# Kernel tuning notes

Hardware: AMD Instinct MI355X
Metric: run time of the kernel (lower is better)

## Reference

```python
import jax, jax.numpy as jnp
import numpy as np

DIM = 512
H = 8
HD = DIM // H
MAX_DIST = 128
TABLE = (2 * MAX_DIST + 1) ** 2
LAMBDA_INIT = 0.8


def setup_inputs() -> dict:
    key = jax.random.key(0)
    ks = jax.random.split(key, 20)
    B, Nq, Nkv = 4, 1024, 1024
    inp = {
        "x_q": jax.random.normal(ks[0], (B, Nq, DIM), jnp.float32),
        "x_kv": jax.random.normal(ks[1], (B, Nkv, DIM), jnp.float32),
        "coords_q": jax.random.randint(ks[2], (B, Nq, 2), 0, 256, jnp.int32),
        "coords_k": jax.random.randint(ks[3], (B, Nkv, 2), 0, 256, jnp.int32),
        "alpha_map": jax.random.uniform(ks[4], (B, Nq, 1), jnp.float32),
        "Wq": jax.random.normal(ks[5], (DIM, DIM), jnp.float32) * 0.02,
        "bq": jnp.zeros((DIM,), jnp.float32),
        "Wk": jax.random.normal(ks[6], (DIM, DIM), jnp.float32) * 0.02,
        "bk": jnp.zeros((DIM,), jnp.float32),
        "Wv": jax.random.normal(ks[7], (DIM, DIM), jnp.float32) * 0.02,
        "bv": jnp.zeros((DIM,), jnp.float32),
        "lambda_q1": jax.random.normal(ks[8], (H // 2, HD), jnp.float32) * 0.1,
        "lambda_k1": jax.random.normal(ks[9], (H // 2, HD), jnp.float32) * 0.1,
        "lambda_q2": jax.random.normal(ks[10], (H // 2, HD), jnp.float32) * 0.1,
        "lambda_k2": jax.random.normal(ks[11], (H // 2, HD), jnp.float32) * 0.1,
        "rpe_table": jax.random.normal(ks[12], (TABLE, H), jnp.float32) * 0.02,
        "Wp": jax.random.normal(ks[13], (DIM, DIM), jnp.float32) * 0.02,
        "bp": jnp.zeros((DIM,), jnp.float32),
    }
    return inp


def reference(x_q, x_kv, coords_q, coords_k, alpha_map,
              Wq, bq, Wk, bk, Wv, bv,
              lambda_q1, lambda_k1, lambda_q2, lambda_k2,
              rpe_table, Wp, bp):
    B, Nq, C = x_q.shape
    Nkv = x_kv.shape[1]
    n_half = H // 2
    scale = HD ** -0.5

    # projections -> [B, H, N, HD]
    q = (x_q @ Wq.T + bq).reshape(B, Nq, H, HD).transpose(0, 2, 1, 3)
    k = (x_kv @ Wk.T + bk).reshape(B, Nkv, H, HD).transpose(0, 2, 1, 3)
    v = (x_kv @ Wv.T + bv).reshape(B, Nkv, H, HD).transpose(0, 2, 1, 3)

    # sparse relative position bias: gather per-pair from table
    rel = coords_q[:, :, None, :] - coords_k[:, None, :, :] + MAX_DIST  # [B,Nq,Nkv,2]
    rel = jnp.clip(rel, 0, 2 * MAX_DIST)
    idx = rel[..., 0] * (2 * MAX_DIST + 1) + rel[..., 1]  # [B,Nq,Nkv]
    bias = rpe_table[idx].transpose(0, 3, 1, 2)  # [B,H,Nq,Nkv]

    scores = jnp.einsum('bhqd,bhkd->bhqk', q, k) * scale + bias
    probs = jax.nn.softmax(scores, axis=-1)
    x_std = jnp.einsum('bhqk,bhkd->bhqd', probs, v)

    lam1 = jnp.exp(jnp.sum(lambda_q1 * lambda_k1, axis=-1))  # [n_half]
    lam2 = jnp.exp(jnp.sum(lambda_q2 * lambda_k2, axis=-1))
    lam = (lam1 - lam2 + LAMBDA_INIT)[None, :, None, None]

    attn_diff = probs[:, :n_half] - lam * probs[:, n_half:]
    x_diff = jnp.einsum('bhqk,bhkd->bhqd', attn_diff, v[:, :n_half])

    alpha = alpha_map[:, None]  # [B,1,Nq,1]
    x1 = x_std[:, :n_half] + alpha * x_diff
    x = jnp.concatenate([x1, x_std[:, n_half:]], axis=1)  # [B,H,Nq,HD]
    x = x.transpose(0, 2, 1, 3).reshape(B, Nq, C)
    return x @ Wp.T + bp
```

## Files before the change

kernel.cpp:

```cpp
#include <hip/hip_runtime.h>
#include <cstddef>
#include <cstdint>

#define DIM   512
#define NSEQ  1024
#define NB    4
#define LOG2E 1.44269504f

typedef unsigned short u16;
typedef short bf16x8 __attribute__((ext_vector_type(8)));
typedef _Float16 half8v __attribute__((ext_vector_type(8)));
typedef float f32x4  __attribute__((ext_vector_type(4)));

#define MFMA(a, b, c)  __builtin_amdgcn_mfma_f32_16x16x32_bf16(a, b, c, 0, 0, 0)
#define MFMAH(a, b, c) __builtin_amdgcn_mfma_f32_16x16x32_f16(a, b, c, 0, 0, 0)

__device__ inline void split2(float x, u16& h, u16& l) {
  unsigned u = __float_as_uint(x);
  unsigned hb = (u + 0x7fffu + ((u >> 16) & 1u)) >> 16;
  float fh = __uint_as_float(hb << 16);
  float r = x - fh;
  unsigned v = __float_as_uint(r);
  unsigned lb = (v + 0x7fffu + ((v >> 16) & 1u)) >> 16;
  h = (u16)hb; l = (u16)lb;
}

__device__ inline uint2 pack4(const u16 a[4]) {
  return make_uint2((unsigned)a[0] | ((unsigned)a[1] << 16),
                    (unsigned)a[2] | ((unsigned)a[3] << 16));
}

__device__ inline u16 f2h(float x) {
  _Float16 h = (_Float16)x;
  u16 r; __builtin_memcpy(&r, &h, 2);
  return r;
}
__device__ inline float h2f(u16 b) {
  _Float16 h; __builtin_memcpy(&h, &b, 2);
  return (float)h;
}
__device__ inline unsigned pkh2(float a, float b) {
  return (unsigned)f2h(a) | ((unsigned)f2h(b) << 16);
}

__device__ inline void split_body(const float* __restrict__ in,
                                  u16* __restrict__ out, int e4) {
  const int e = e4 * 4;
  const int m = e >> 9, c = e & 511;
  const float4 v = *(const float4*)(in + e);
  u16 h[4], l[4];
  split2(v.x, h[0], l[0]); split2(v.y, h[1], l[1]);
  split2(v.z, h[2], l[2]); split2(v.w, h[3], l[3]);
  u16* o = out + (size_t)m * 1024 + c;
  *(uint2*)o = pack4(h);
  *(uint2*)(o + 512) = pack4(l);
}

#define GLDS(g, l)                                                        \
  __builtin_amdgcn_global_load_lds(                                       \
      (const __attribute__((address_space(1))) void*)(g),                 \
      (__attribute__((address_space(3))) void*)(l), 16, 0, 0)

__global__ __launch_bounds__(256) void prep(
    const float* __restrict__ wq, const float* __restrict__ wk,
    const float* __restrict__ wv, const float* __restrict__ wp,
    const float* __restrict__ xq, const float* __restrict__ xkv,
    const int* __restrict__ cq, const int* __restrict__ ck,
    const float* __restrict__ rpe,
    u16* __restrict__ w2, u16* __restrict__ xq2, u16* __restrict__ xkv2,
    u16* __restrict__ biasT) {
  __shared__ u16 Ts[8 * 16 * 64];
  const int id = blockIdx.x;
  const int t = threadIdx.x;
  if (id < 1024) {
    const int y = id >> 8;
    const float* src = (y == 0) ? wq : (y == 1) ? wk : (y == 2) ? wv : wp;
    split_body(src, w2 + (size_t)y * 524288, (id & 255) * 256 + t);
  } else if (id < 5120) {
    const int e = id - 1024;
    const int y = e >> 11;
    split_body(y ? xkv : xq, y ? xkv2 : xq2, (e & 2047) * 256 + t);
  } else {
    const int e = id - 5120;
    const int q0 = (e & 15) * 64, k0 = ((e >> 4) & 63) * 16, b = e >> 10;
    const int qn = t & 63, kb = t >> 6;
    const int2 cqv = ((const int2*)cq)[b * NSEQ + q0 + qn];
#pragma unroll
    for (int j = 0; j < 4; ++j) {
      const int k = kb * 4 + j;
      const int2 ckv = ((const int2*)ck)[b * NSEQ + k0 + k];
      const int r0 = min(max(cqv.x - ckv.x + 128, 0), 256);
      const int r1 = min(max(cqv.y - ckv.y + 128, 0), 256);
      const float* rp = rpe + (size_t)(r0 * 257 + r1) * 8;
      const float4 f0 = *(const float4*)rp;
      const float4 f1 = *(const float4*)(rp + 4);
      u16* dst = Ts + k * 64 + qn;
      dst[0 * 1024] = f2h(f0.x * LOG2E); dst[1 * 1024] = f2h(f0.y * LOG2E);
      dst[2 * 1024] = f2h(f0.z * LOG2E); dst[3 * 1024] = f2h(f0.w * LOG2E);
      dst[4 * 1024] = f2h(f1.x * LOG2E); dst[5 * 1024] = f2h(f1.y * LOG2E);
      dst[6 * 1024] = f2h(f1.z * LOG2E); dst[7 * 1024] = f2h(f1.w * LOG2E);
    }
    __syncthreads();
#pragma unroll
    for (int i = 0; i < 4; ++i) {
      const int e2 = i * 256 + t;
      const int row = e2 >> 3, c8 = e2 & 7;
      const int hh = row >> 4, k = row & 15;
      const uint4 v = *(const uint4*)(Ts + row * 64 + c8 * 8);
      *(uint4*)(biasT + ((size_t)(b * 8 + hh) * 1024 + k0 + k) * 1024 +
                q0 + c8 * 8) = v;
    }
  }
}

template <int OUT_MODE>
__device__ __forceinline__ void gemm128(
    u16* __restrict__ Ah, u16* __restrict__ Al,
    u16* __restrict__ Bh, u16* __restrict__ Bl,
    const u16* __restrict__ A2, const u16* __restrict__ B2,
    const float* __restrict__ bias, void* __restrict__ outp,
    float scale, int m0, int n0) {
  const int tid = threadIdx.x;
  const int lane = tid & 63, w = tid >> 6;
  const int wm = (w & 1) * 64, wn = (w >> 1) * 32;
  const int lr = lane >> 3;
  const int scc = (lane & 7) ^ lr;

  const u16* gA = A2 + (size_t)(m0 + w * 32 + lr) * 1024 + scc * 8;
  const u16* gB = B2 + (size_t)(n0 + w * 16 + lr) * 1024 + scc * 8;
  char* lAh = (char*)Ah + w * 4096;  char* lAl = (char*)Al + w * 4096;
  char* lBh = (char*)Bh + w * 2048;  char* lBl = (char*)Bl + w * 2048;

  const int fr = lane & 15, kq = lane >> 4, fx = fr & 7;
  int aoff[2][4], boff[2][2];
#pragma unroll
  for (int s = 0; s < 2; ++s) {
#pragma unroll
    for (int i = 0; i < 4; ++i)
      aoff[s][i] = (wm + i * 16 + fr) * 64 + (((s * 4 + kq) ^ fx)) * 8;
#pragma unroll
    for (int j = 0; j < 2; ++j)
      boff[s][j] = (wn + j * 16 + fr) * 64 + (((s * 4 + kq) ^ fx)) * 8;
  }

  f32x4 acc[4][2] = {};
  for (int k0 = 0; k0 < 512; k0 += 64) {
    __syncthreads();
#pragma unroll
    for (int i = 0; i < 4; ++i) {
      GLDS(gA + (size_t)i * 8192 + k0, lAh + i * 1024);
      GLDS(gA + (size_t)i * 8192 + 512 + k0, lAl + i * 1024);
    }
#pragma unroll
    for (int i = 0; i < 2; ++i) {
      GLDS(gB + (size_t)i * 8192 + k0, lBh + i * 1024);
      GLDS(gB + (size_t)i * 8192 + 512 + k0, lBl + i * 1024);
    }
    __syncthreads();
#pragma unroll
    for (int s = 0; s < 2; ++s) {
      bf16x8 ah[4], al[4], bh[2], bl[2];
#pragma unroll
      for (int i = 0; i < 4; ++i) {
        ah[i] = *(const bf16x8*)(Ah + aoff[s][i]);
        al[i] = *(const bf16x8*)(Al + aoff[s][i]);
      }
#pragma unroll
      for (int j = 0; j < 2; ++j) {
        bh[j] = *(const bf16x8*)(Bh + boff[s][j]);
        bl[j] = *(const bf16x8*)(Bl + boff[s][j]);
      }
#pragma unroll
      for (int i = 0; i < 4; ++i)
#pragma unroll
        for (int j = 0; j < 2; ++j) {
          acc[i][j] = MFMA(al[i], bh[j], acc[i][j]);
          acc[i][j] = MFMA(ah[i], bl[j], acc[i][j]);
          acc[i][j] = MFMA(ah[i], bh[j], acc[i][j]);
        }
    }
  }

  const int er = (lane >> 4) * 4, ec = lane & 15;
#pragma unroll
  for (int i = 0; i < 4; ++i)
#pragma unroll
    for (int j = 0; j < 2; ++j) {
      const int row = m0 + wm + i * 16 + er;
      const int col = n0 + wn + j * 16 + ec;
      const float bv = bias[col];
      if (OUT_MODE == 4) {
        u16 hf[4];
#pragma unroll
        for (int r = 0; r < 4; ++r) hf[r] = f2h((acc[i][j][r] + bv) * scale);
        const int bb = row >> 10, kk = row & 1023;
        *(uint2*)((u16*)outp + ((size_t)(bb * 512 + col)) * 1024 + kk) =
            pack4(hf);
      } else {
#pragma unroll
        for (int r = 0; r < 4; ++r) {
          const float v = (acc[i][j][r] + bv) * scale;
          if (OUT_MODE == 3)
            ((u16*)outp)[(size_t)(row + r) * 512 + col] = f2h(v);
          else
            ((float*)outp)[(size_t)(row + r) * 512 + col] = v;
        }
      }
    }
}

__global__ __launch_bounds__(256, 3) void gemm_qkv(
    const u16* __restrict__ xq2, const u16* __restrict__ xkv2,
    const u16* __restrict__ w2, const float* __restrict__ bq,
    const float* __restrict__ bk, const float* __restrict__ bv,
    u16* __restrict__ q2f, u16* __restrict__ k2f, u16* __restrict__ vtf) {
  __shared__ __align__(16) u16 Ah[8192], Al[8192], Bh[4096], Bl[4096];
  const int z = blockIdx.z;
  const int m0 = blockIdx.x * 128, n0 = blockIdx.y * 64;
  if (z == 0)
    gemm128<3>(Ah, Al, Bh, Bl, xq2, w2, bq, q2f, 0.125f * LOG2E, m0, n0);
  else if (z == 1)
    gemm128<3>(Ah, Al, Bh, Bl, xkv2, w2 + 524288, bk, k2f, 1.0f, m0, n0);
  else
    gemm128<4>(Ah, Al, Bh, Bl, xkv2, w2 + 2 * 524288, bv, vtf, 1.0f, m0, n0);
}

__global__ __launch_bounds__(256, 3) void gemm_out(
    const u16* __restrict__ xa2, const u16* __restrict__ w2p,
    const float* __restrict__ bp, float* __restrict__ out) {
  __shared__ __align__(16) u16 Ah[8192], Al[8192], Bh[4096], Bl[4096];
  gemm128<0>(Ah, Al, Bh, Bl, xa2, w2p, bp, out, 1.0f,
             blockIdx.x * 128, blockIdx.y * 64);
}

__global__ __launch_bounds__(256) void attn_f16(
    const u16* __restrict__ q2f, const u16* __restrict__ k2f,
    const u16* __restrict__ vtf, const float* __restrict__ amap,
    const float* __restrict__ lq1, const float* __restrict__ lk1,
    const float* __restrict__ lq2, const float* __restrict__ lk2,
    const u16* __restrict__ biasT, u16* __restrict__ xo) {
  __shared__ __align__(16) u16 KsL[2][8192];
  __shared__ __align__(16) u16 VtL[2][8192];
  __shared__ float lam_s;

  const int tid = threadIdx.x;
  const int lane = tid & 63, w = tid >> 6;
  const int h = w >> 1, qs = w & 1;
  const int hp = blockIdx.y, b = blockIdx.z;
  const int q0 = blockIdx.x * 32;
  const int head = hp + 4 * h;
  const int lq = lane & 15, lg = lane >> 4;
  const int q = qs * 16 + lq;
  const size_t qrow = (size_t)(b * NSEQ + q0 + q);

  if (tid < 64) {
    float p1 = lq1[hp * 64 + tid] * lk1[hp * 64 + tid];
    float p2 = lq2[hp * 64 + tid] * lk2[hp * 64 + tid];
#pragma unroll
    for (int m = 32; m >= 1; m >>= 1) {
      p1 += __shfl_xor(p1, m, 64);
      p2 += __shfl_xor(p2, m, 64);
    }
    if (tid == 0) lam_s = __expf(p1) - __expf(p2) + 0.8f;
  }

  const float alpha = amap[qrow];

  half8v Qf[2];
#pragma unroll
  for (int ks = 0; ks < 2; ++ks)
    Qf[ks] = *(const half8v*)(q2f + qrow * 512 + head * 64 + ks * 32 + lg * 8);

  f32x4 Ya[4] = {};
  f32x4 Yb[4] = {};
  float m_run = -1e30f, l_run = 0.0f;

  const int lr = lane >> 3;
  const int scc = (lane & 7) ^ lr;
  const int cw = w * 4;

  auto stage = [&](int it, int p) {
#pragma unroll
    for (int i = 0; i < 4; ++i) {
      const int c = cw + i;
      const int row = c * 8 + lr;
      const int sh = row >> 6, k = row & 63;
      const u16* src = k2f + (size_t)(b * NSEQ + it * 64 + k) * 512 +
                       (hp + 4 * sh) * 64 + scc * 8;
      GLDS(src, (char*)KsL[p] + c * 1024);
    }
#pragma unroll
    for (int i = 0; i < 4; ++i) {
      const int c = cw + i;
      const int row = c * 8 + lr;
      const int hv = row >> 6, d = row & 63;
      const u16* src = vtf + (size_t)(b * 512 + (hp + 4 * hv) * 64 + d) * 1024 +
                       it * 64 + scc * 8;
      GLDS(src, (char*)VtL[p] + c * 1024);
    }
  };

  const u16* bT = biasT + ((size_t)(b * 8 + head) << 20) + q0 + q;
  auto loadBias = [&](int it, u16* rb) {
    const u16* bt = bT + (size_t)(it * 64) * 1024;
#pragma unroll
    for (int kt = 0; kt < 4; ++kt)
#pragma unroll
      for (int r = 0; r < 4; ++r)
        rb[kt * 4 + r] = bt[(size_t)(kt * 16 + lg * 4 + r) * 1024];
  };

  u16 rbA[16], rbB[16];
  stage(0, 0);
  loadBias(0, rbA);

  auto body = [&](int it, u16* rbCur, u16* rbNext) {
    const int p = it & 1;
    __syncthreads();
    if (it + 1 < 16) { stage(it + 1, p ^ 1); loadBias(it + 1, rbNext); }

    const u16* Kb = KsL[p];
    f32x4 st[4] = {};
#pragma unroll
    for (int kt = 0; kt < 4; ++kt) {
      const int krow = kt * 16 + lq;
      const int rx = krow & 7;
#pragma unroll
      for (int ks = 0; ks < 2; ++ks) {
        const int phys = (ks * 4 + lg) ^ rx;
        const half8v kf =
            *(const half8v*)(Kb + (h * 64 + krow) * 64 + phys * 8);
        st[kt] = MFMAH(kf, Qf[ks], st[kt]);
      }
    }

    float sv[4][4];
    float mx = -1e30f;
#pragma unroll
    for (int kt = 0; kt < 4; ++kt)
#pragma unroll
      for (int r = 0; r < 4; ++r) {
        const float s = st[kt][r] + h2f(rbCur[kt * 4 + r]);
        sv[kt][r] = s;
        mx = fmaxf(mx, s);
      }
    mx = fmaxf(mx, __shfl_xor(mx, 16, 64));
    mx = fmaxf(mx, __shfl_xor(mx, 32, 64));
    const float mnew = fmaxf(m_run, mx);
    const float a = exp2f(m_run - mnew);
    m_run = mnew;
    float pr[4][4], ps = 0.0f;
#pragma unroll
    for (int kt = 0; kt < 4; ++kt)
#pragma unroll
      for (int r = 0; r < 4; ++r) {
        pr[kt][r] = exp2f(sv[kt][r] - mnew);
        ps += pr[kt][r];
      }
    ps += __shfl_xor(ps, 16, 64);
    ps += __shfl_xor(ps, 32, 64);
    l_run = l_run * a + ps;
#pragma unroll
    for (int dt = 0; dt < 4; ++dt) Ya[dt] *= a;
    if (h == 1) {
#pragma unroll
      for (int dt = 0; dt < 4; ++dt) Yb[dt] *= a;
    }

    unsigned pk[4][2];
#pragma unroll
    for (int kt = 0; kt < 4; ++kt) {
      pk[kt][0] = pkh2(pr[kt][0], pr[kt][1]);
      pk[kt][1] = pkh2(pr[kt][2], pr[kt][3]);
    }
    const int srcA = lq + ((lg & 1) << 5);
    const bool t2 = lg >= 2;
    half8v pb[2];
#pragma unroll
    for (int kg = 0; kg < 2; ++kg) {
      const int k0i = kg * 2, k1i = kg * 2 + 1;
      const unsigned A0 = __shfl((int)pk[k0i][0], srcA);
      const unsigned A1 = __shfl((int)pk[k0i][1], srcA);
      const unsigned B0 = __shfl((int)pk[k1i][0], srcA);
      const unsigned B1 = __shfl((int)pk[k1i][1], srcA);
      const unsigned C0 = __shfl((int)pk[k0i][0], srcA + 16);
      const unsigned C1 = __shfl((int)pk[k0i][1], srcA + 16);
      const unsigned D0 = __shfl((int)pk[k1i][0], srcA + 16);
      const unsigned D1 = __shfl((int)pk[k1i][1], srcA + 16);
      const uint4 Pu = make_uint4(t2 ? B0 : A0, t2 ? B1 : A1,
                                  t2 ? D0 : C0, t2 ? D1 : C1);
      __builtin_memcpy(&pb[kg], &Pu, 16);
    }

    const u16* Vb = VtL[p];
#pragma unroll
    for (int kg = 0; kg < 2; ++kg) {
      if (h == 0) {
#pragma unroll
        for (int dt = 0; dt < 4; ++dt) {
          const int d = dt * 16 + lq;
          const int phys = (kg * 4 + lg) ^ (d & 7);
          const half8v v1 = *(const half8v*)(Vb + d * 64 + phys * 8);
          Ya[dt] = MFMAH(v1, pb[kg], Ya[dt]);
        }
      } else {
#pragma unroll
        for (int dt = 0; dt < 4; ++dt) {
          const int d = dt * 16 + lq;
          const int phys = (kg * 4 + lg) ^ (d & 7);
          const half8v v1 = *(const half8v*)(Vb + d * 64 + phys * 8);
          Yb[dt] = MFMAH(v1, pb[kg], Yb[dt]);
          const half8v v2 = *(const half8v*)(Vb + (64 + d) * 64 + phys * 8);
          Ya[dt] = MFMAH(v2, pb[kg], Ya[dt]);
        }
      }
    }
  };

  for (int it2 = 0; it2 < 16; it2 += 2) {
    body(it2, rbA, rbB);
    body(it2 + 1, rbB, rbA);
  }

  __syncthreads();
  float* y2x = (float*)VtL;
  float* l2s = (float*)KsL;
  if (h == 1) {
    if (lane < 16) l2s[qs * 16 + lane] = l_run;
#pragma unroll
    for (int dt = 0; dt < 4; ++dt)
#pragma unroll
      for (int r = 0; r < 4; ++r)
        y2x[(qs * 64 + lane) * 16 + dt * 4 + r] = Yb[dt][r];
  }
  __syncthreads();
  if (h == 1) {
    const float inv2 = 1.0f / l_run;
#pragma unroll
    for (int dt = 0; dt < 4; ++dt) {
      u16 hh[4], ll[4];
#pragma unroll
      for (int r = 0; r < 4; ++r) split2(Ya[dt][r] * inv2, hh[r], ll[r]);
      u16* o = xo + qrow * 1024 + (hp + 4) * 64 + dt * 16 + lg * 4;
      *(uint2*)o = pack4(hh);
      *(uint2*)(o + 512) = pack4(ll);
    }
  } else {
    const float inv1 = 1.0f / l_run;
    const float inv2 = 1.0f / l2s[qs * 16 + lq];
    const float c1 = (1.0f + alpha) * inv1;
    const float c2 = alpha * lam_s * inv2;
#pragma unroll
    for (int dt = 0; dt < 4; ++dt) {
      u16 hh[4], ll[4];
#pragma unroll
      for (int r = 0; r < 4; ++r) {
        const float y2 = y2x[(qs * 64 + lane) * 16 + dt * 4 + r];
        split2(c1 * Ya[dt][r] - c2 * y2, hh[r], ll[r]);
      }
      u16* o = xo + qrow * 1024 + hp * 64 + dt * 16 + lg * 4;
      *(uint2*)o = pack4(hh);
      *(uint2*)(o + 512) = pack4(ll);
    }
  }
}

extern "C" void kernel_launch(void* const* d_in, const int* in_sizes, int n_in,
                              void* d_out, int out_size, void* d_ws, size_t ws_size,
                              hipStream_t stream) {
  const float* x_q   = (const float*)d_in[0];
  const float* x_kv  = (const float*)d_in[1];
  const int*   c_q   = (const int*)d_in[2];
  const int*   c_k   = (const int*)d_in[3];
  const float* alpha = (const float*)d_in[4];
  const float* Wq    = (const float*)d_in[5];
  const float* bq    = (const float*)d_in[6];
  const float* Wk    = (const float*)d_in[7];
  const float* bk    = (const float*)d_in[8];
  const float* Wv    = (const float*)d_in[9];
  const float* bv    = (const float*)d_in[10];
  const float* lq1   = (const float*)d_in[11];
  const float* lk1   = (const float*)d_in[12];
  const float* lq2   = (const float*)d_in[13];
  const float* lk2   = (const float*)d_in[14];
  const float* rpe   = (const float*)d_in[15];
  const float* Wp    = (const float*)d_in[16];
  const float* bp    = (const float*)d_in[17];

  u16* w2    = (u16*)d_ws;
  u16* xq2   = (u16*)((char*)d_ws + (4u << 20));
  u16* q2f   = (u16*)((char*)d_ws + (12u << 20));
  u16* k2f   = (u16*)((char*)d_ws + (16u << 20));
  u16* vtf   = (u16*)((char*)d_ws + (20u << 20));
  u16* xa    = xq2;
  u16* biasT = (u16*)((char*)d_ws + (28u << 20));
  u16* xkv2  = (u16*)d_out;

  prep<<<9216, 256, 0, stream>>>(Wq, Wk, Wv, Wp, x_q, x_kv, c_q, c_k, rpe,
                                 w2, xq2, xkv2, biasT);
  gemm_qkv<<<dim3(32, 8, 3), 256, 0, stream>>>(xq2, xkv2, w2, bq, bk, bv,
                                               q2f, k2f, vtf);
  attn_f16<<<dim3(32, 4, NB), 256, 0, stream>>>(
      q2f, k2f, vtf, alpha, lq1, lk1, lq2, lk2, biasT, xa);
  gemm_out<<<dim3(32, 8), 256, 0, stream>>>(xa, w2 + 3 * 524288, bp,
                                            (float*)d_out);
}
```

Baseline: 210.3 us.

## Split attention KV range across two warp groups with flash-decode style merge

The attention kernel doubles its block to 512 threads and gives each half of the key sequence to a separate group of four waves. Each group runs online softmax over 32-key tiles, and the partial max, sum and output accumulators are then merged through shared memory before the final differential combine. The aim is more waves per block to hide latency and a shorter serial loop per wave. In exchange it adds a merge step with extra syncs, and it drops the bias register prefetch, so bias loads now happen inside each iteration.

```diff
diff --git a/kernel.cpp b/kernel.cpp
--- a/kernel.cpp
+++ b/kernel.cpp
@@ -233,19 +233,22 @@
              blockIdx.x * 128, blockIdx.y * 64);
 }
 
-__global__ __launch_bounds__(256) void attn_f16(
+__global__ __launch_bounds__(512) void attn_f16(
     const u16* __restrict__ q2f, const u16* __restrict__ k2f,
     const u16* __restrict__ vtf, const float* __restrict__ amap,
     const float* __restrict__ lq1, const float* __restrict__ lk1,
     const float* __restrict__ lq2, const float* __restrict__ lk2,
     const u16* __restrict__ biasT, u16* __restrict__ xo) {
-  __shared__ __align__(16) u16 KsL[2][8192];
-  __shared__ __align__(16) u16 VtL[2][8192];
+  __shared__ __align__(16) u16 KsL[2][2][4096];
+  __shared__ __align__(16) u16 VtL[2][2][4096];
+  __shared__ float2 mls[2][2][2][16];
+  __shared__ float l2s[32];
   __shared__ float lam_s;
 
   const int tid = threadIdx.x;
   const int lane = tid & 63, w = tid >> 6;
-  const int h = w >> 1, qs = w & 1;
+  const int kg = w >> 2, h = (w >> 1) & 1, qs = w & 1;
+  const int wl = w & 3;
   const int hp = blockIdx.y, b = blockIdx.z;
   const int q0 = blockIdx.x * 32;
   const int head = hp + 4 * h;
@@ -276,71 +279,71 @@
   float m_run = -1e30f, l_run = 0.0f;
 
   const int lr = lane >> 3;
-  const int scc = (lane & 7) ^ lr;
-  const int cw = w * 4;
+  const int lc = (lane & 7) ^ lr;
+  const int cw = wl * 2;
 
   auto stage = [&](int it, int p) {
-#pragma unroll
-    for (int i = 0; i < 4; ++i) {
+    const int kbase = kg * 512 + it * 32;
+#pragma unroll
+    for (int i = 0; i < 2; ++i) {
       const int c = cw + i;
       const int row = c * 8 + lr;
-      const int sh = row >> 6, k = row & 63;
-      const u16* src = k2f + (size_t)(b * NSEQ + it * 64 + k) * 512 +
-                       (hp + 4 * sh) * 64 + scc * 8;
-      GLDS(src, (char*)KsL[p] + c * 1024);
-    }
-#pragma unroll
-    for (int i = 0; i < 4; ++i) {
+      const int sh = row >> 5, k = row & 31;
+      const u16* src = k2f + (size_t)(b * NSEQ + kbase + k) * 512 +
+                       (hp + 4 * sh) * 64 + lc * 8;
+      GLDS(src, (char*)KsL[kg][p] + c * 1024);
+    }
+#pragma unroll
+    for (int i = 0; i < 2; ++i) {
       const int c = cw + i;
-      const int row = c * 8 + lr;
-      const int hv = row >> 6, d = row & 63;
+      const int d = c * 8 + lr;
+      const int hv = lc >> 2, kc = lc & 3;
       const u16* src = vtf + (size_t)(b * 512 + (hp + 4 * hv) * 64 + d) * 1024 +
-                       it * 64 + scc * 8;
-      GLDS(src, (char*)VtL[p] + c * 1024);
+                       kbase + kc * 8;
+      GLDS(src, (char*)VtL[kg][p] + c * 1024);
     }
   };
 
   const u16* bT = biasT + ((size_t)(b * 8 + head) << 20) + q0 + q;
-  auto loadBias = [&](int it, u16* rb) {
-    const u16* bt = bT + (size_t)(it * 64) * 1024;
-#pragma unroll
-    for (int kt = 0; kt < 4; ++kt)
-#pragma unroll
-      for (int r = 0; r < 4; ++r)
-        rb[kt * 4 + r] = bt[(size_t)(kt * 16 + lg * 4 + r) * 1024];
-  };
-
-  u16 rbA[16], rbB[16];
+
   stage(0, 0);
-  loadBias(0, rbA);
-
-  auto body = [&](int it, u16* rbCur, u16* rbNext) {
+
+  for (int it = 0; it < 16; ++it) {
     const int p = it & 1;
     __syncthreads();
-    if (it + 1 < 16) { stage(it + 1, p ^ 1); loadBias(it + 1, rbNext); }
-
-    const u16* Kb = KsL[p];
-    f32x4 st[4] = {};
-#pragma unroll
-    for (int kt = 0; kt < 4; ++kt) {
+    if (it + 1 < 16) stage(it + 1, p ^ 1);
+
+    u16 rb[8];
+    {
+      const u16* bt = bT + (size_t)(kg * 512 + it * 32) * 1024;
+#pragma unroll
+      for (int kt = 0; kt < 2; ++kt)
+#pragma unroll
+        for (int r = 0; r < 4; ++r)
+          rb[kt * 4 + r] = bt[(size_t)(kt * 16 + lg * 4 + r) * 1024];
+    }
+
+    const u16* Kb = KsL[kg][p];
+    f32x4 st[2] = {};
+#pragma unroll
+    for (int kt = 0; kt < 2; ++kt) {
       const int krow = kt * 16 + lq;
       const int rx = krow & 7;
 #pragma unroll
       for (int ks = 0; ks < 2; ++ks) {
         const int phys = (ks * 4 + lg) ^ rx;
-        const half8v kf =
-            *(const half8v*)(Kb + (h * 64 + krow) * 64 + phys * 8);
+        const half8v kf = *(const half8v*)(Kb + (h * 32 + krow) * 64 + phys * 8);
         st[kt] = MFMAH(kf, Qf[ks], st[kt]);
       }
     }
 
-    float sv[4][4];
+    float sv[2][4];
     float mx = -1e30f;
 #pragma unroll
-    for (int kt = 0; kt < 4; ++kt)
+    for (int kt = 0; kt < 2; ++kt)
 #pragma unroll
       for (int r = 0; r < 4; ++r) {
-        const float s = st[kt][r] + h2f(rbCur[kt * 4 + r]);
+        const float s = st[kt][r] + h2f(rb[kt * 4 + r]);
         sv[kt][r] = s;
         mx = fmaxf(mx, s);
       }
@@ -349,9 +352,9 @@
     const float mnew = fmaxf(m_run, mx);
     const float a = exp2f(m_run - mnew);
     m_run = mnew;
-    float pr[4][4], ps = 0.0f;
-#pragma unroll
-    for (int kt = 0; kt < 4; ++kt)
+    float pr[2][4], ps = 0.0f;
+#pragma unroll
+    for (int kt = 0; kt < 2; ++kt)
 #pragma unroll
       for (int r = 0; r < 4; ++r) {
         pr[kt][r] = exp2f(sv[kt][r] - mnew);
@@ -367,66 +370,88 @@
       for (int dt = 0; dt < 4; ++dt) Yb[dt] *= a;
     }
 
-    unsigned pk[4][2];
-#pragma unroll
-    for (int kt = 0; kt < 4; ++kt) {
-      pk[kt][0] = pkh2(pr[kt][0], pr[kt][1]);
-      pk[kt][1] = pkh2(pr[kt][2], pr[kt][3]);
-    }
+    const unsigned a0 = pkh2(pr[0][0], pr[0][1]);
+    const unsigned a1 = pkh2(pr[0][2], pr[0][3]);
+    const unsigned b0 = pkh2(pr[1][0], pr[1][1]);
+    const unsigned b1 = pkh2(pr[1][2], pr[1][3]);
     const int srcA = lq + ((lg & 1) << 5);
+    const unsigned A0 = __shfl((int)a0, srcA),      A1 = __shfl((int)a1, srcA);
+    const unsigned B0 = __shfl((int)b0, srcA),      B1 = __shfl((int)b1, srcA);
+    const unsigned C0 = __shfl((int)a0, srcA + 16), C1 = __shfl((int)a1, srcA + 16);
+    const unsigned D0 = __shfl((int)b0, srcA + 16), D1 = __shfl((int)b1, srcA + 16);
     const bool t2 = lg >= 2;
-    half8v pb[2];
-#pragma unroll
-    for (int kg = 0; kg < 2; ++kg) {
-      const int k0i = kg * 2, k1i = kg * 2 + 1;
-      const unsigned A0 = __shfl((int)pk[k0i][0], srcA);
-      const unsigned A1 = __shfl((int)pk[k0i][1], srcA);
-      const unsigned B0 = __shfl((int)pk[k1i][0], srcA);
-      const unsigned B1 = __shfl((int)pk[k1i][1], srcA);
-      const unsigned C0 = __shfl((int)pk[k0i][0], srcA + 16);
-      const unsigned C1 = __shfl((int)pk[k0i][1], srcA + 16);
-      const unsigned D0 = __shfl((int)pk[k1i][0], srcA + 16);
-      const unsigned D1 = __shfl((int)pk[k1i][1], srcA + 16);
-      const uint4 Pu = make_uint4(t2 ? B0 : A0, t2 ? B1 : A1,
-                                  t2 ? D0 : C0, t2 ? D1 : C1);
-      __builtin_memcpy(&pb[kg], &Pu, 16);
-    }
-
-    const u16* Vb = VtL[p];
-#pragma unroll
-    for (int kg = 0; kg < 2; ++kg) {
-      if (h == 0) {
-#pragma unroll
-        for (int dt = 0; dt < 4; ++dt) {
-          const int d = dt * 16 + lq;
-          const int phys = (kg * 4 + lg) ^ (d & 7);
-          const half8v v1 = *(const half8v*)(Vb + d * 64 + phys * 8);
-          Ya[dt] = MFMAH(v1, pb[kg], Ya[dt]);
-        }
-      } else {
-#pragma unroll
-        for (int dt = 0; dt < 4; ++dt) {
-          const int d = dt * 16 + lq;
-          const int phys = (kg * 4 + lg) ^ (d & 7);
-          const half8v v1 = *(const half8v*)(Vb + d * 64 + phys * 8);
-          Yb[dt] = MFMAH(v1, pb[kg], Yb[dt]);
-          const half8v v2 = *(const half8v*)(Vb + (64 + d) * 64 + phys * 8);
-          Ya[dt] = MFMAH(v2, pb[kg], Ya[dt]);
-        }
-      }
-    }
-  };
-
-  for (int it2 = 0; it2 < 16; it2 += 2) {
-    body(it2, rbA, rbB);
-    body(it2 + 1, rbB, rbA);
-  }
-
+    const uint4 Pu = make_uint4(t2 ? B0 : A0, t2 ? B1 : A1,
+                                t2 ? D0 : C0, t2 ? D1 : C1);
+    half8v pb;
+    __builtin_memcpy(&pb, &Pu, 16);
+
+    const u16* Vb = VtL[kg][p];
+    if (h == 0) {
+#pragma unroll
+      for (int dt = 0; dt < 4; ++dt) {
+        const int d = dt * 16 + lq;
+        const half8v v1 = *(const half8v*)(Vb + d * 64 + ((lg ^ (d & 7))) * 8);
+        Ya[dt] = MFMAH(v1, pb, Ya[dt]);
+      }
+    } else {
+#pragma unroll
+      for (int dt = 0; dt < 4; ++dt) {
+        const int d = dt * 16 + lq;
+        const int dx = d & 7;
+        const half8v v1 = *(const half8v*)(Vb + d * 64 + ((lg ^ dx)) * 8);
+        Yb[dt] = MFMAH(v1, pb, Yb[dt]);
+        const half8v v2 = *(const half8v*)(Vb + d * 64 + (((4 + lg) ^ dx)) * 8);
+        Ya[dt] = MFMAH(v2, pb, Ya[dt]);
+      }
+    }
+  }
+
+  float* mY = (float*)KsL;
+  float* mB = (float*)VtL;
   __syncthreads();
-  float* y2x = (float*)VtL;
-  float* l2s = (float*)KsL;
-  if (h == 1) {
-    if (lane < 16) l2s[qs * 16 + lane] = l_run;
+  if (lane < 16) mls[kg][h][qs][lane] = make_float2(m_run, l_run);
+  if (kg == 1) {
+#pragma unroll
+    for (int dt = 0; dt < 4; ++dt)
+#pragma unroll
+      for (int r = 0; r < 4; ++r)
+        mY[((h * 2 + qs) * 64 + lane) * 16 + dt * 4 + r] = Ya[dt][r];
+    if (h == 1) {
+#pragma unroll
+      for (int dt = 0; dt < 4; ++dt)
+#pragma unroll
+        for (int r = 0; r < 4; ++r)
+          mB[(qs * 64 + lane) * 16 + dt * 4 + r] = Yb[dt][r];
+    }
+  }
+  __syncthreads();
+  float l_tot = l_run;
+  if (kg == 0) {
+    const float2 o = mls[1][h][qs][lq];
+    const float mm = fmaxf(m_run, o.x);
+    const float s0 = exp2f(m_run - mm);
+    const float s1 = exp2f(o.x - mm);
+    l_tot = l_run * s0 + o.y * s1;
+    const float* sY = mY + ((h * 2 + qs) * 64 + lane) * 16;
+#pragma unroll
+    for (int dt = 0; dt < 4; ++dt)
+#pragma unroll
+      for (int r = 0; r < 4; ++r)
+        Ya[dt][r] = Ya[dt][r] * s0 + sY[dt * 4 + r] * s1;
+    if (h == 1) {
+      const float* sB = mB + (qs * 64 + lane) * 16;
+#pragma unroll
+      for (int dt = 0; dt < 4; ++dt)
+#pragma unroll
+        for (int r = 0; r < 4; ++r)
+          Yb[dt][r] = Yb[dt][r] * s0 + sB[dt * 4 + r] * s1;
+    }
+  }
+
+  __syncthreads();
+  float* y2x = (float*)KsL;
+  if (kg == 0 && h == 1) {
+    if (lane < 16) l2s[qs * 16 + lane] = l_tot;
 #pragma unroll
     for (int dt = 0; dt < 4; ++dt)
 #pragma unroll
@@ -434,8 +459,8 @@
         y2x[(qs * 64 + lane) * 16 + dt * 4 + r] = Yb[dt][r];
   }
   __syncthreads();
-  if (h == 1) {
-    const float inv2 = 1.0f / l_run;
+  if (kg == 0 && h == 1) {
+    const float inv2 = 1.0f / l_tot;
 #pragma unroll
     for (int dt = 0; dt < 4; ++dt) {
       u16 hh[4], ll[4];
@@ -445,8 +470,8 @@
       *(uint2*)o = pack4(hh);
       *(uint2*)(o + 512) = pack4(ll);
     }
-  } else {
-    const float inv1 = 1.0f / l_run;
+  } else if (kg == 0 && h == 0) {
+    const float inv1 = 1.0f / l_tot;
     const float inv2 = 1.0f / l2s[qs * 16 + lq];
     const float c1 = (1.0f + alpha) * inv1;
     const float c2 = alpha * lam_s * inv2;
@@ -500,7 +525,7 @@
                                  w2, xq2, xkv2, biasT);
   gemm_qkv<<<dim3(32, 8, 3), 256, 0, stream>>>(xq2, xkv2, w2, bq, bk, bv,
                                                q2f, k2f, vtf);
-  attn_f16<<<dim3(32, 4, NB), 256, 0, stream>>>(
+  attn_f16<<<dim3(32, 4, NB), 512, 0, stream>>>(
       q2f, k2f, vtf, alpha, lq1, lk1, lq2, lk2, biasT, xa);
   gemm_out<<<dim3(32, 8), 256, 0, stream>>>(xa, w2 + 3 * 524288, bp,
                                             (float*)d_out);
```

After: 207.0 us. Within noise of the previous version (-1.5%).
